# Kernel tuning notes

Measured on AMD Instinct MI355X. Metric: run time of the kernel, lower is better.

The kernel has to match this reference:

```python
import jax, jax.numpy as jnp
import numpy as np

NUM_TYPES = 16
D_IN = 256
D_OUT = 256
N = 262144


def setup_inputs() -> dict:
    key = jax.random.key(0)
    k_x, k_idx, k_w = jax.random.split(key, 3)
    x = jax.random.normal(k_x, (N, D_IN), dtype=jnp.float32)
    idx = jax.random.randint(k_idx, (N,), 0, NUM_TYPES, dtype=jnp.int64)
    # One weight matrix per type; e3nn-style normalization 1/sqrt(d_in)
    W = jax.random.normal(k_w, (NUM_TYPES, D_IN, D_OUT), dtype=jnp.float32) / jnp.sqrt(
        jnp.float32(D_IN)
    )
    return {"x": x, "idx": idx, "W": W}


def reference(x, idx, W):
    # Per-element indexed linear: out[n] = x[n] @ W[idx[n]].
    # Avoid gathering a [N, d_in, d_out] weight tensor: mask inputs per type
    # and run one dense GEMM per type (T is a small fixed constant).
    num_types = W.shape[0]
    out = jnp.zeros((x.shape[0], W.shape[-1]), dtype=x.dtype)
    for t in range(num_types):
        mask = (idx == t).astype(x.dtype)[:, None]  # [N, 1]
        out = out + (x * mask) @ W[t]
    return out
```

## Files before the change

### kernel.cpp

```cpp
#include <hip/hip_runtime.h>
#include <hip/hip_bf16.h>


#define NTYPES 16
#define GRID_BLOCKS 256

typedef __bf16 bf16x8 __attribute__((ext_vector_type(8)));
typedef float f32x4 __attribute__((ext_vector_type(4)));

static __device__ __forceinline__ unsigned int f2bf_pk(float a, float b) {
  unsigned int ua = __float_as_uint(a);
  unsigned int ub = __float_as_uint(b);
  ua = (ua + 0x7FFFu + ((ua >> 16) & 1u)) >> 16;
  ub = (ub + 0x7FFFu + ((ub >> 16) & 1u)) >> 16;
  return ua | (ub << 16);
}

static __device__ __forceinline__ unsigned int cvtpk(float a, float b) {
  unsigned int r;
  asm("v_cvt_pk_bf16_f32 %0, %1, %2" : "=v"(r) : "v"(a), "v"(b));
  return r;
}


__global__ void zero_meta_kernel(unsigned int* meta) {
  if (threadIdx.x < 128) meta[threadIdx.x] = 0;
}

__global__ void hist_kernel(const int* __restrict__ idx, int N,
                            unsigned int* __restrict__ meta) {
  __shared__ unsigned int h[NTYPES];
  if (threadIdx.x < NTYPES) h[threadIdx.x] = 0;
  __syncthreads();
  for (int n = blockIdx.x * 256 + threadIdx.x; n < N; n += gridDim.x * 256)
    atomicAdd(&h[idx[n] & 15], 1u);
  __syncthreads();
  if (threadIdx.x < NTYPES) atomicAdd(&meta[threadIdx.x], h[threadIdx.x]);
}

__global__ void prefix_kernel(unsigned int* meta) {
  if (threadIdx.x == 0) {
    unsigned int o = 0;
    for (int t = 0; t < NTYPES; t++) {
      meta[16 + t] = o;
      meta[32 + t] = o;
      o += meta[t];
    }
  }
}

__global__ void scatter_kernel(const int* __restrict__ idx, int N,
                               unsigned int* __restrict__ meta,
                               int* __restrict__ perm) {
  __shared__ unsigned int h[NTYPES];
  __shared__ unsigned int base[NTYPES];
  int b0 = blockIdx.x * 4096;
  if (threadIdx.x < NTYPES) h[threadIdx.x] = 0;
  __syncthreads();
  unsigned int lr[16];
  int tt[16];
#pragma unroll
  for (int i = 0; i < 16; i++) {
    int n = b0 + i * 256 + threadIdx.x;
    int t = (n < N) ? (idx[n] & 15) : 0;
    tt[i] = t;
    lr[i] = (n < N) ? atomicAdd(&h[t], 1u) : 0u;
  }
  __syncthreads();
  if (threadIdx.x < NTYPES)
    base[threadIdx.x] = atomicAdd(&meta[32 + threadIdx.x], h[threadIdx.x]);
  __syncthreads();
#pragma unroll
  for (int i = 0; i < 16; i++) {
    int n = b0 + i * 256 + threadIdx.x;
    if (n < N) perm[base[tt[i]] + lr[i]] = n;
  }
}

__global__ void packW_kernel(const float* __restrict__ W,
                             unsigned short* __restrict__ Wp) {
  int id = blockIdx.x * 256 + threadIdx.x;
  int c = id & 255;
  int tk = id >> 8;
  const float* src = W + (size_t)tk * 32 * 256 + c;
  unsigned int buf[16];
#pragma unroll
  for (int p = 0; p < 16; p++)
    buf[p] = f2bf_pk(src[(2 * p) * 256], src[(2 * p + 1) * 256]);
  uint4* d4 = (uint4*)(Wp + (size_t)id * 32);
#pragma unroll
  for (int p = 0; p < 4; p++)
    d4[p] = make_uint4(buf[4 * p], buf[4 * p + 1], buf[4 * p + 2], buf[4 * p + 3]);
}

__global__ __launch_bounds__(512, 2) void gemm_kernel(
    const float* __restrict__ x, const unsigned short* __restrict__ Wp,
    const int* __restrict__ perm, const unsigned int* __restrict__ meta,
    float* __restrict__ out, float* __restrict__ dump, int N) {
  __shared__ uint4 Wlds4[8192];

  int b = blockIdx.x;
  int t = b >> 4;
  int s = b & 15;
  unsigned int off = meta[16 + t];
  unsigned int cnt = meta[t];

  int tid = threadIdx.x;
  int l = tid & 63, w = tid >> 6;
  int lm = l & 15, lh = l >> 4;

  const uint4* Wp4 = (const uint4*)Wp;
  for (int f = w; f < 128; f += 8) {
    int kk = f >> 4, fn = f & 15;
    Wlds4[f * 64 + l] =
        Wp4[(size_t)((t * 8 + kk) * 256 + fn * 16 + lm) * 4 + lh];
  }
  __syncthreads();

  int Tt = (int)((cnt + 15u) >> 4);
  int lo = (s * Tt) >> 4;
  int hi = ((s + 1) * Tt) >> 4;

  int nmask = N - 1;
  float* dumpP = dump + (size_t)tid * 4;

  int j = lo + w;
  if (j >= hi) return;

  float4 xb[16];
  int prow, ps0, ps1, ps2, ps3;
  {
    unsigned int rowbase = off + (unsigned)j * 16u;
    prow = perm[rowbase + lm] & nmask;
    ps0 = perm[rowbase + lh * 4 + 0];
    ps1 = perm[rowbase + lh * 4 + 1];
    ps2 = perm[rowbase + lh * 4 + 2];
    ps3 = perm[rowbase + lh * 4 + 3];
    const float4* xr = (const float4*)x + (size_t)prow * 64 + lh * 2;
#pragma unroll
    for (int kk = 0; kk < 8; kk++) {
      xb[2 * kk] = xr[kk * 8];
      xb[2 * kk + 1] = xr[kk * 8 + 1];
    }
  }
  asm volatile("s_waitcnt vmcnt(0)" ::: "memory");

  for (; j < hi; j += 8) {
    int rem = (int)cnt - j * 16;
    int nrows = rem < 16 ? rem : 16;
    int myps[4];
    myps[0] = ps0 & nmask;
    myps[1] = ps1 & nmask;
    myps[2] = ps2 & nmask;
    myps[3] = ps3 & nmask;

    bf16x8 afr[8];
#pragma unroll
    for (int kk = 0; kk < 8; kk++) {
      uint4 v;
      v.x = cvtpk(xb[2 * kk].x, xb[2 * kk].y);
      v.y = cvtpk(xb[2 * kk].z, xb[2 * kk].w);
      v.z = cvtpk(xb[2 * kk + 1].x, xb[2 * kk + 1].y);
      v.w = cvtpk(xb[2 * kk + 1].z, xb[2 * kk + 1].w);
      afr[kk] = __builtin_bit_cast(bf16x8, v);
    }

    int jn = j + 8;
    if (jn < hi) {
      unsigned int rowbase = off + (unsigned)jn * 16u;
      prow = perm[rowbase + lm] & nmask;
      ps0 = perm[rowbase + lh * 4 + 0];
      ps1 = perm[rowbase + lh * 4 + 1];
      ps2 = perm[rowbase + lh * 4 + 2];
      ps3 = perm[rowbase + lh * 4 + 3];
      const float4* xr = (const float4*)x + (size_t)prow * 64 + lh * 2;
#pragma unroll
      for (int kk = 0; kk < 8; kk++) {
        xb[2 * kk] = xr[kk * 8];
        xb[2 * kk + 1] = xr[kk * 8 + 1];
      }
    }
    __builtin_amdgcn_sched_barrier(0);

    f32x4 acc[16];
#pragma unroll
    for (int fn = 0; fn < 16; fn++) acc[fn] = (f32x4){0.f, 0.f, 0.f, 0.f};
#pragma unroll
    for (int kk = 0; kk < 8; kk++) {
#pragma unroll
      for (int fn = 0; fn < 16; fn++) {
        bf16x8 bb = __builtin_bit_cast(bf16x8, Wlds4[(kk * 16 + fn) * 64 + l]);
        acc[fn] = __builtin_amdgcn_mfma_f32_16x16x32_bf16(afr[kk], bb,
                                                          acc[fn], 0, 0, 0);
      }
    }

#pragma unroll
    for (int fn = 0; fn < 16; fn++) {
#pragma unroll
      for (int r_ = 0; r_ < 4; r_++) {
        int rit = lh * 4 + r_;
        bool valid = rit < nrows;
        float* p = valid
                       ? out + (size_t)myps[r_] * 256 + fn * 16 + lm
                       : dumpP + r_;
        *p = acc[fn][r_];
      }
    }

    asm volatile("s_waitcnt vmcnt(48)" ::: "memory");
  }
}

extern "C" void kernel_launch(void* const* d_in, const int* in_sizes, int n_in,
                              void* d_out, int out_size, void* d_ws,
                              size_t ws_size, hipStream_t stream) {
  const float* x = (const float*)d_in[0];
  const int* idx = (const int*)d_in[1];
  const float* W = (const float*)d_in[2];
  float* out = (float*)d_out;
  int N = in_sizes[0] / 256;

  unsigned int* meta = (unsigned int*)d_ws;
  float* dump = (float*)((char*)d_ws + 512);
  int* perm = (int*)((char*)d_ws + 512 + 65536);
  unsigned short* Wp =
      (unsigned short*)((char*)d_ws + 512 + 65536 + (size_t)N * 4 + 128);

  zero_meta_kernel<<<1, 128, 0, stream>>>(meta);
  hist_kernel<<<256, 256, 0, stream>>>(idx, N, meta);
  prefix_kernel<<<1, 64, 0, stream>>>(meta);
  packW_kernel<<<128, 256, 0, stream>>>(W, Wp);
  int nScatter = (N + 4095) / 4096;
  scatter_kernel<<<nScatter, 256, 0, stream>>>(idx, N, meta, perm);

  gemm_kernel<<<GRID_BLOCKS, 512, 0, stream>>>(x, Wp, perm, meta, out, dump,
                                               N);
}
```

Before: 140.3 us.

## Swap MFMA operands to store output rows as float4 and prefetch perm further ahead

Swaps the A/B operands of the MFMA so each lane's accumulator holds four consecutive output columns of one row. The epilogue can then write float4 stores to a single row instead of 64 scalar scattered stores across four rows. The perm index for the next-next tile is now loaded one iteration ahead, so only one perm load per lane is needed. The vmcnt wait drops from 48 to 16 to match the smaller number of outstanding stores, which adds risk if that count is wrong.

```diff
diff --git a/kernel.cpp b/kernel.cpp
--- a/kernel.cpp
+++ b/kernel.cpp
@@ -128,31 +128,23 @@
   if (j >= hi) return;
 
   float4 xb[16];
-  int prow, ps0, ps1, ps2, ps3;
+  int prowCur, prowNext = 0;
   {
-    unsigned int rowbase = off + (unsigned)j * 16u;
-    prow = perm[rowbase + lm] & nmask;
-    ps0 = perm[rowbase + lh * 4 + 0];
-    ps1 = perm[rowbase + lh * 4 + 1];
-    ps2 = perm[rowbase + lh * 4 + 2];
-    ps3 = perm[rowbase + lh * 4 + 3];
-    const float4* xr = (const float4*)x + (size_t)prow * 64 + lh * 2;
+    prowCur = perm[off + (unsigned)j * 16u + lm] & nmask;
+    const float4* xr = (const float4*)x + (size_t)prowCur * 64 + lh * 2;
 #pragma unroll
     for (int kk = 0; kk < 8; kk++) {
       xb[2 * kk] = xr[kk * 8];
       xb[2 * kk + 1] = xr[kk * 8 + 1];
     }
+    if (j + 8 < hi) prowNext = perm[off + (unsigned)(j + 8) * 16u + lm] & nmask;
   }
   asm volatile("s_waitcnt vmcnt(0)" ::: "memory");
 
   for (; j < hi; j += 8) {
     int rem = (int)cnt - j * 16;
     int nrows = rem < 16 ? rem : 16;
-    int myps[4];
-    myps[0] = ps0 & nmask;
-    myps[1] = ps1 & nmask;
-    myps[2] = ps2 & nmask;
-    myps[3] = ps3 & nmask;
+    int prowSt = prowCur;
 
     bf16x8 afr[8];
 #pragma unroll
@@ -167,19 +159,16 @@
 
     int jn = j + 8;
     if (jn < hi) {
-      unsigned int rowbase = off + (unsigned)jn * 16u;
-      prow = perm[rowbase + lm] & nmask;
-      ps0 = perm[rowbase + lh * 4 + 0];
-      ps1 = perm[rowbase + lh * 4 + 1];
-      ps2 = perm[rowbase + lh * 4 + 2];
-      ps3 = perm[rowbase + lh * 4 + 3];
-      const float4* xr = (const float4*)x + (size_t)prow * 64 + lh * 2;
+      const float4* xr = (const float4*)x + (size_t)prowNext * 64 + lh * 2;
 #pragma unroll
       for (int kk = 0; kk < 8; kk++) {
         xb[2 * kk] = xr[kk * 8];
         xb[2 * kk + 1] = xr[kk * 8 + 1];
       }
     }
+    int prowNext2 = 0;
+    if (j + 16 < hi)
+      prowNext2 = perm[off + (unsigned)(j + 16) * 16u + lm] & nmask;
     __builtin_amdgcn_sched_barrier(0);
 
     f32x4 acc[16];
@@ -190,25 +179,25 @@
 #pragma unroll
       for (int fn = 0; fn < 16; fn++) {
         bf16x8 bb = __builtin_bit_cast(bf16x8, Wlds4[(kk * 16 + fn) * 64 + l]);
-        acc[fn] = __builtin_amdgcn_mfma_f32_16x16x32_bf16(afr[kk], bb,
+        acc[fn] = __builtin_amdgcn_mfma_f32_16x16x32_bf16(bb, afr[kk],
                                                           acc[fn], 0, 0, 0);
       }
     }
 
-#pragma unroll
-    for (int fn = 0; fn < 16; fn++) {
-#pragma unroll
-      for (int r_ = 0; r_ < 4; r_++) {
-        int rit = lh * 4 + r_;
-        bool valid = rit < nrows;
-        float* p = valid
-                       ? out + (size_t)myps[r_] * 256 + fn * 16 + lm
-                       : dumpP + r_;
-        *p = acc[fn][r_];
+    {
+      bool valid = lm < nrows;
+      float* orow = out + (size_t)prowSt * 256 + lh * 4;
+#pragma unroll
+      for (int fn = 0; fn < 16; fn++) {
+        float* p = valid ? orow + fn * 16 : dumpP;
+        *(float4*)p = __builtin_bit_cast(float4, acc[fn]);
       }
     }
 
-    asm volatile("s_waitcnt vmcnt(48)" ::: "memory");
+    asm volatile("s_waitcnt vmcnt(16)" ::: "memory");
+
+    prowCur = prowNext;
+    prowNext = prowNext2;
   }
 }
 
```

Result: no change. 142.6 us (+1.7%).
